# Performance work log

Measured on AMD Instinct MI355X. Metric: run time of the kernel, lower is better.

Reference implementation:

```python
import jax, jax.numpy as jnp
import numpy as np

N_NODES = 100000
N_EDGES = 1600000
C_IN, C_HID, C_OUT = 32, 32, 8
N_AGENTS = 1000


def _glorot(key, shape):
    fan_in, fan_out = shape[0], shape[1]
    lim = float(np.sqrt(6.0 / (fan_in + fan_out)))
    return jax.random.uniform(key, shape, jnp.float32, -lim, lim)


def setup_inputs() -> dict:
    key = jax.random.key(0)
    ks = jax.random.split(key, 16)
    x = jax.random.normal(ks[0], (N_NODES, C_IN), jnp.float32)
    edge_index = jax.random.randint(ks[1], (2, N_EDGES), 0, N_NODES, jnp.int64)
    d = {"x": x, "edge_index": edge_index}
    dims = [(C_IN, C_HID), (C_HID, C_HID), (C_HID, C_HID)]
    for i, (di, do) in enumerate(dims, start=1):
        d[f"W_l{i}"] = _glorot(ks[2 * i], (di, do))        # neighbor (aggregated) weight
        d[f"b_l{i}"] = jnp.zeros((do,), jnp.float32)
        d[f"W_r{i}"] = _glorot(ks[2 * i + 1], (di, do))    # root/self weight (no bias)
    d["W_out"] = _glorot(ks[10], (C_HID, C_OUT))
    d["b_out"] = jnp.zeros((C_OUT,), jnp.float32)
    return d


def _sage_conv(x, src, dst, W_l, b_l, W_r):
    # mean-aggregate neighbor features at destination nodes
    msg = x[src]                                               # [E, d] gather
    summed = jax.ops.segment_sum(msg, dst, num_segments=N_NODES)
    cnt = jax.ops.segment_sum(jnp.ones((src.shape[0],), x.dtype), dst,
                              num_segments=N_NODES)
    agg = summed / jnp.maximum(cnt, 1.0)[:, None]              # deg==0 -> 0
    return agg @ W_l + b_l + x @ W_r


def reference(x, edge_index, W_l1, b_l1, W_r1, W_l2, b_l2, W_r2,
              W_l3, b_l3, W_r3, W_out, b_out):
    src, dst = edge_index[0], edge_index[1]
    h = jax.nn.relu(_sage_conv(x, src, dst, W_l1, b_l1, W_r1))
    h = jax.nn.relu(_sage_conv(h, src, dst, W_l2, b_l2, W_r2))
    h = jax.nn.relu(_sage_conv(h, src, dst, W_l3, b_l3, W_r3))
    out = h @ W_out + b_out
    return out[:N_AGENTS]
```

## Files before the change

kernel.cpp:

```cpp
#include <hip/hip_runtime.h>
#include <hip/hip_bf16.h>

#define N_NODES 100000
#define N_EDGES 1600000
#define N_AGENTS 1000

#define NB 782
#define ABLK 512
#define CHUNK (N_EDGES / ABLK)
#define CONV_BLOCKS 3125

typedef short s16x8 __attribute__((ext_vector_type(8)));
typedef float f32x4 __attribute__((ext_vector_type(4)));

__device__ __forceinline__ unsigned short f2bf(float f) {
    unsigned u = __float_as_uint(f);
    u += 0x7fffu + ((u >> 16) & 1u);
    return (unsigned short)(u >> 16);
}
__device__ __forceinline__ float bflo(unsigned u) { return __uint_as_float(u << 16); }
__device__ __forceinline__ float bfhi(unsigned u) { return __uint_as_float(u & 0xffff0000u); }

__global__ __launch_bounds__(256) void hist_prep_kernel(
    const int* __restrict__ dst, int* __restrict__ partialT,
    const float* __restrict__ x, unsigned short* __restrict__ xb,
    const float* __restrict__ Wl1, const float* __restrict__ Wr1,
    const float* __restrict__ Wl2, const float* __restrict__ Wr2,
    const float* __restrict__ Wl3, const float* __restrict__ Wr3,
    unsigned short* __restrict__ Wcat)
{
    int b = blockIdx.x;
    if (b < ABLK) {
        __shared__ int hist[NB];
        for (int i = threadIdx.x; i < NB; i += 256) hist[i] = 0;
        __syncthreads();
        int beg = b * CHUNK;
        for (int e = beg + threadIdx.x; e < beg + CHUNK; e += 256)
            atomicAdd(&hist[dst[e] >> 7], 1);
        __syncthreads();
        for (int i = threadIdx.x; i < NB; i += 256) partialT[i * ABLK + b] = hist[i];
    } else if (b < ABLK + CONV_BLOCKS) {
        int i = (b - ABLK) * 256 + threadIdx.x;
        float4 v = ((const float4*)x)[i];
        ((ushort4*)xb)[i] = make_ushort4(f2bf(v.x), f2bf(v.y), f2bf(v.z), f2bf(v.w));
    } else {
        int gid = (b - ABLK - CONV_BLOCKS) * 256 + threadIdx.x;
        if (gid >= 3 * 2048) return;
        int L = gid >> 11, idx = gid & 2047;
        int k = idx >> 5, n = idx & 31;
        const float* Wl = (L == 0) ? Wl1 : (L == 1) ? Wl2 : Wl3;
        const float* Wr = (L == 0) ? Wr1 : (L == 1) ? Wr2 : Wr3;
        float v = (k < 32) ? Wl[k * 32 + n] : Wr[(k - 32) * 32 + n];
        Wcat[gid] = f2bf(v);
    }
}

__global__ __launch_bounds__(256) void bucket_prefix_kernel(
    const int* __restrict__ partialT, int* __restrict__ baseT, int* __restrict__ tot)
{
    int wave = threadIdx.x >> 6, lane = threadIdx.x & 63;
    int t = blockIdx.x * 4 + wave;
    if (t >= NB) return;
    const int4* p = (const int4*)(partialT + (size_t)t * ABLK);
    int4 u0 = p[lane * 2], u1 = p[lane * 2 + 1];
    int v0 = u0.x, v1 = u0.y, v2 = u0.z, v3 = u0.w;
    int v4 = u1.x, v5 = u1.y, v6 = u1.z, v7 = u1.w;
    int p0 = 0, p1 = v0, p2 = p1 + v1, p3 = p2 + v2;
    int p4 = p3 + v3, p5 = p4 + v4, p6 = p5 + v5, p7 = p6 + v6;
    int s = p7 + v7;
    int x = s;
    #pragma unroll
    for (int off = 1; off < 64; off <<= 1) {
        int y = __shfl_up(x, off);
        if (lane >= off) x += y;
    }
    int excl = x - s;
    int4* q = (int4*)(baseT + (size_t)t * ABLK);
    q[lane * 2]     = make_int4(excl + p0, excl + p1, excl + p2, excl + p3);
    q[lane * 2 + 1] = make_int4(excl + p4, excl + p5, excl + p6, excl + p7);
    if (lane == 63) tot[t] = x;
}

__global__ __launch_bounds__(1024) void total_scan_kernel(
    const int* __restrict__ tot, int* __restrict__ bstart)
{
    __shared__ int tmp[1024];
    int t = threadIdx.x;
    int v = (t < NB) ? tot[t] : 0;
    tmp[t] = v;
    __syncthreads();
    for (int off = 1; off < 1024; off <<= 1) {
        int u = (t >= off) ? tmp[t - off] : 0;
        __syncthreads();
        tmp[t] += u;
        __syncthreads();
    }
    if (t < NB) {
        bstart[t] = tmp[t] - v;
        if (t == NB - 1) bstart[NB] = tmp[t];
    }
}

__global__ __launch_bounds__(256) void bucket_scatter_kernel(
    const int* __restrict__ src, const int* __restrict__ dst,
    const int* __restrict__ baseT, const int* __restrict__ bstart,
    int* __restrict__ ebuf)
{
    __shared__ int cur[NB];
    int b = blockIdx.x;
    for (int i = threadIdx.x; i < NB; i += 256)
        cur[i] = bstart[i] + baseT[(size_t)i * ABLK + b];
    __syncthreads();
    int beg = b * CHUNK;
    for (int e = beg + threadIdx.x; e < beg + CHUNK; e += 256) {
        int d = dst[e];
        int slot = atomicAdd(&cur[d >> 7], 1);
        ebuf[slot] = src[e] | ((d & 127) << 17);
    }
}

__global__ __launch_bounds__(256) void bucket_csr_kernel(
    const int* __restrict__ bstart, const int* __restrict__ ebuf,
    int* __restrict__ rowptr, float* __restrict__ inv, int* __restrict__ esrc)
{
    __shared__ int hist[128], cur[128], tmp[256];
    int b = blockIdx.x;
    int t = threadIdx.x;
    int beg = bstart[b], end = bstart[b + 1];
    if (t < 128) hist[t] = 0;
    __syncthreads();
    for (int i = beg + t; i < end; i += 256)
        atomicAdd(&hist[(ebuf[i] >> 17) & 127], 1);
    __syncthreads();
    int v = (t < 128) ? hist[t] : 0;
    tmp[t] = v;
    __syncthreads();
    for (int off = 1; off < 256; off <<= 1) {
        int u = (t >= off) ? tmp[t - off] : 0;
        __syncthreads();
        tmp[t] += u;
        __syncthreads();
    }
    int excl = tmp[t] - v;
    int node = b * 128 + t;
    if (t < 128 && node < N_NODES) {
        rowptr[node] = beg + excl;
        inv[node] = 1.0f / fmaxf((float)v, 1.0f);
        cur[t] = beg + excl;
    }
    if (b == NB - 1 && t == 0) rowptr[N_NODES] = N_EDGES;
    __syncthreads();
    for (int i = beg + t; i < end; i += 256) {
        int p = ebuf[i];
        int slot = atomicAdd(&cur[(p >> 17) & 127], 1);
        esrc[slot] = p & 0x1FFFF;
    }
}

__global__ __launch_bounds__(256) void sage_fused_kernel(
    const int* __restrict__ rowptr, const int* __restrict__ esrc,
    const float* __restrict__ inv, const unsigned short* __restrict__ hb,
    const unsigned short* __restrict__ Wcat, const float* __restrict__ bl,
    const float* __restrict__ Wout, const float* __restrict__ bout,
    void* __restrict__ outp, int n_nodes, int final)
{
    __shared__ unsigned short sW[2048];
    __shared__ float sb[32];
    __shared__ unsigned short smean[64 * 40];
    __shared__ float sh3[64 * 33];
    __shared__ float sWo[256];
    __shared__ float sbo[8];

    int tid = threadIdx.x;
    ((uint4*)sW)[tid] = ((const uint4*)Wcat)[tid];
    if (tid < 32) sb[tid] = bl[tid];
    if (final) {
        sWo[tid] = Wout[tid];
        if (tid < 8) sbo[tid] = bout[tid];
    }

    int lane = tid & 63, wave = tid >> 6;

    int g = lane >> 2, q = lane & 3;
    int nodeA = blockIdx.x * 64 + wave * 16 + g;
    int beg = 0, end = 0;
    if (nodeA < n_nodes) { beg = rowptr[nodeA]; end = rowptr[nodeA + 1]; }
    float a0 = 0.f, a1 = 0.f, a2 = 0.f, a3 = 0.f;
    float a4 = 0.f, a5 = 0.f, a6 = 0.f, a7 = 0.f;
    int j = beg;
    for (; j + 1 < end; j += 2) {
        int s0 = esrc[j];
        int s1 = esrc[j + 1];
        uint4 u0 = *(const uint4*)(hb + s0 * 32 + q * 8);
        uint4 u1 = *(const uint4*)(hb + s1 * 32 + q * 8);
        a0 += bflo(u0.x); a1 += bfhi(u0.x);
        a2 += bflo(u0.y); a3 += bfhi(u0.y);
        a4 += bflo(u0.z); a5 += bfhi(u0.z);
        a6 += bflo(u0.w); a7 += bfhi(u0.w);
        a0 += bflo(u1.x); a1 += bfhi(u1.x);
        a2 += bflo(u1.y); a3 += bfhi(u1.y);
        a4 += bflo(u1.z); a5 += bfhi(u1.z);
        a6 += bflo(u1.w); a7 += bfhi(u1.w);
    }
    if (j < end) {
        int s = esrc[j];
        uint4 u = *(const uint4*)(hb + s * 32 + q * 8);
        a0 += bflo(u.x); a1 += bfhi(u.x);
        a2 += bflo(u.y); a3 += bfhi(u.y);
        a4 += bflo(u.z); a5 += bfhi(u.z);
        a6 += bflo(u.w); a7 += bfhi(u.w);
    }
    float iv = (nodeA < n_nodes) ? inv[nodeA] : 0.f;
    uint4 o;
    o.x = (unsigned)f2bf(a0 * iv) | ((unsigned)f2bf(a1 * iv) << 16);
    o.y = (unsigned)f2bf(a2 * iv) | ((unsigned)f2bf(a3 * iv) << 16);
    o.z = (unsigned)f2bf(a4 * iv) | ((unsigned)f2bf(a5 * iv) << 16);
    o.w = (unsigned)f2bf(a6 * iv) | ((unsigned)f2bf(a7 * iv) << 16);
    int mrow = wave * 16 + g;
    *(uint4*)&smean[mrow * 40 + q * 8] = o;
    __syncthreads();

    int l15 = lane & 15, quad = lane >> 4;
    s16x8 bf_[2][2];
    #pragma unroll
    for (int kt = 0; kt < 2; kt++)
        #pragma unroll
        for (int nt = 0; nt < 2; nt++)
            #pragma unroll
            for (int jj = 0; jj < 8; jj++) {
                int k = kt * 32 + quad * 8 + jj;
                bf_[kt][nt][jj] = (short)sW[k * 32 + l15 + nt * 16];
            }
    float bias0 = sb[l15], bias1 = sb[l15 + 16];

    int tilebase = blockIdx.x * 64 + wave * 16;
    int nodeD = tilebase + l15;
    int na = min(nodeD, n_nodes - 1);
    s16x8 am = *(const s16x8*)&smean[(wave * 16 + l15) * 40 + quad * 8];
    s16x8 as = *(const s16x8*)(hb + (size_t)na * 32 + quad * 8);
    f32x4 acc0 = {0.f, 0.f, 0.f, 0.f};
    f32x4 acc1 = {0.f, 0.f, 0.f, 0.f};
    acc0 = __builtin_amdgcn_mfma_f32_16x16x32_bf16(am, bf_[0][0], acc0, 0, 0, 0);
    acc0 = __builtin_amdgcn_mfma_f32_16x16x32_bf16(as, bf_[1][0], acc0, 0, 0, 0);
    acc1 = __builtin_amdgcn_mfma_f32_16x16x32_bf16(am, bf_[0][1], acc1, 0, 0, 0);
    acc1 = __builtin_amdgcn_mfma_f32_16x16x32_bf16(as, bf_[1][1], acc1, 0, 0, 0);

    if (!final) {
        #pragma unroll
        for (int r = 0; r < 4; r++) {
            int onode = tilebase + quad * 4 + r;
            if (onode < n_nodes) {
                ((unsigned short*)outp)[onode * 32 + l15]      = f2bf(fmaxf(acc0[r] + bias0, 0.f));
                ((unsigned short*)outp)[onode * 32 + l15 + 16] = f2bf(fmaxf(acc1[r] + bias1, 0.f));
            }
        }
    } else {
        #pragma unroll
        for (int r = 0; r < 4; r++) {
            int row = wave * 16 + quad * 4 + r;
            sh3[row * 33 + l15]      = fmaxf(acc0[r] + bias0, 0.f);
            sh3[row * 33 + l15 + 16] = fmaxf(acc1[r] + bias1, 0.f);
        }
        __syncthreads();
        #pragma unroll
        for (int i = tid; i < 512; i += 256) {
            int ln = i >> 3, c = i & 7;
            int gn = blockIdx.x * 64 + ln;
            if (gn < N_AGENTS) {
                float ov = sbo[c];
                #pragma unroll
                for (int k = 0; k < 32; k++) ov += sh3[ln * 33 + k] * sWo[k * 8 + c];
                ((float*)outp)[gn * 8 + c] = ov;
            }
        }
    }
}

extern "C" void kernel_launch(void* const* d_in, const int* in_sizes, int n_in,
                              void* d_out, int out_size, void* d_ws, size_t ws_size,
                              hipStream_t stream) {
    const float* x   = (const float*)d_in[0];
    const int* ei    = (const int*)d_in[1];
    const float* Wl1 = (const float*)d_in[2];
    const float* bl1 = (const float*)d_in[3];
    const float* Wr1 = (const float*)d_in[4];
    const float* Wl2 = (const float*)d_in[5];
    const float* bl2 = (const float*)d_in[6];
    const float* Wr2 = (const float*)d_in[7];
    const float* Wl3 = (const float*)d_in[8];
    const float* bl3 = (const float*)d_in[9];
    const float* Wr3 = (const float*)d_in[10];
    const float* Wout = (const float*)d_in[11];
    const float* bout = (const float*)d_in[12];
    float* out = (float*)d_out;

    const int* src = ei;
    const int* dst = ei + N_EDGES;

    char* ws = (char*)d_ws;
    int*   rowptr   = (int*)ws;                                ws += (size_t)(N_NODES + 8) * 4;
    float* inv      = (float*)ws;                              ws += (size_t)N_NODES * 4;
    int*   partialT = (int*)ws;                                ws += (size_t)NB * ABLK * 4;
    int*   baseT    = (int*)ws;                                ws += (size_t)NB * ABLK * 4;
    int*   tot      = (int*)ws;                                ws += 784 * 4;
    int*   bstart   = (int*)ws;                                ws += 784 * 4;
    int*   esrc     = (int*)ws;                                ws += (size_t)N_EDGES * 4;
    unsigned short* hXb   = (unsigned short*)ws;               ws += (size_t)N_NODES * 32 * 2;
    unsigned short* hAb   = (unsigned short*)ws;               ws += (size_t)N_NODES * 32 * 2;
    unsigned short* hBb   = (unsigned short*)ws;               ws += (size_t)N_NODES * 32 * 2;
    unsigned short* Wcat  = (unsigned short*)ws;               ws += 3 * 2048 * 2;
    int*   ebuf     = (int*)hAb;

    hist_prep_kernel<<<ABLK + CONV_BLOCKS + 24, 256, 0, stream>>>(
        dst, partialT, x, hXb, Wl1, Wr1, Wl2, Wr2, Wl3, Wr3, Wcat);
    bucket_prefix_kernel<<<(NB + 3) / 4, 256, 0, stream>>>(partialT, baseT, tot);
    total_scan_kernel<<<1, 1024, 0, stream>>>(tot, bstart);
    bucket_scatter_kernel<<<ABLK, 256, 0, stream>>>(src, dst, baseT, bstart, ebuf);
    bucket_csr_kernel<<<NB, 256, 0, stream>>>(bstart, ebuf, rowptr, inv, esrc);

    sage_fused_kernel<<<(N_NODES + 63) / 64, 256, 0, stream>>>(
        rowptr, esrc, inv, hXb, Wcat, bl1, Wout, bout, hAb, N_NODES, 0);
    sage_fused_kernel<<<(N_NODES + 63) / 64, 256, 0, stream>>>(
        rowptr, esrc, inv, hAb, Wcat + 2048, bl2, Wout, bout, hBb, N_NODES, 0);
    sage_fused_kernel<<<(N_AGENTS + 63) / 64, 256, 0, stream>>>(
        rowptr, esrc, inv, hBb, Wcat + 4096, bl3, Wout, bout, out, N_AGENTS, 1);
}
```

Baseline: 213.1 us.

## Sort nodes by in-degree to balance per-wave edge loops in SAGE layers

Builds a per-bucket degree histogram in the CSR kernel, scans it, and computes a permutation of nodes ordered by descending degree (capped at 63). The first two SAGE layers process nodes in this permuted order, so the 16 nodes in a wave have similar edge counts, reducing divergence and idle lanes in the gather loop. In exchange it adds two extra kernel launches and an indirection load, scatters output writes to non-contiguous rows, and lowers locality of the self-feature loads.

```diff
diff --git a/kernel.cpp b/kernel.cpp
--- a/kernel.cpp
+++ b/kernel.cpp
@@ -121,13 +121,15 @@
 
 __global__ __launch_bounds__(256) void bucket_csr_kernel(
     const int* __restrict__ bstart, const int* __restrict__ ebuf,
-    int* __restrict__ rowptr, float* __restrict__ inv, int* __restrict__ esrc)
-{
-    __shared__ int hist[128], cur[128], tmp[256];
+    int* __restrict__ rowptr, float* __restrict__ inv, int* __restrict__ esrc,
+    int* __restrict__ dbinP)
+{
+    __shared__ int hist[128], cur[128], tmp[256], dhist[64];
     int b = blockIdx.x;
     int t = threadIdx.x;
     int beg = bstart[b], end = bstart[b + 1];
     if (t < 128) hist[t] = 0;
+    if (t < 64) dhist[t] = 0;
     __syncthreads();
     for (int i = beg + t; i < end; i += 256)
         atomicAdd(&hist[(ebuf[i] >> 17) & 127], 1);
@@ -147,14 +149,71 @@
         rowptr[node] = beg + excl;
         inv[node] = 1.0f / fmaxf((float)v, 1.0f);
         cur[t] = beg + excl;
+        atomicAdd(&dhist[min(v, 63)], 1);
     }
     if (b == NB - 1 && t == 0) rowptr[N_NODES] = N_EDGES;
     __syncthreads();
+    if (t < 64) dbinP[b * 64 + t] = dhist[t];
     for (int i = beg + t; i < end; i += 256) {
         int p = ebuf[i];
         int slot = atomicAdd(&cur[(p >> 17) & 127], 1);
         esrc[slot] = p & 0x1FFFF;
     }
+}
+
+__global__ __launch_bounds__(256) void deg_scan_kernel(
+    const int* __restrict__ dbinP, int* __restrict__ dbaseP, int* __restrict__ dtot)
+{
+    int wave = threadIdx.x >> 6, lane = threadIdx.x & 63;
+    int bin = blockIdx.x * 4 + wave;
+    int vals[13];
+    int s = 0;
+    #pragma unroll
+    for (int it = 0; it < 13; it++) {
+        int b = lane * 13 + it;
+        int v = (b < NB) ? dbinP[b * 64 + bin] : 0;
+        vals[it] = v; s += v;
+    }
+    int x = s;
+    #pragma unroll
+    for (int off = 1; off < 64; off <<= 1) {
+        int y = __shfl_up(x, off);
+        if (lane >= off) x += y;
+    }
+    int run = x - s;
+    #pragma unroll
+    for (int it = 0; it < 13; it++) {
+        int b = lane * 13 + it;
+        if (b < NB) dbaseP[b * 64 + bin] = run;
+        run += vals[it];
+    }
+    if (lane == 63) dtot[bin] = x;
+}
+
+__global__ __launch_bounds__(256) void perm_place_kernel(
+    const int* __restrict__ rowptr, const int* __restrict__ dbinP,
+    const int* __restrict__ dbaseP, const int* __restrict__ dtot,
+    int* __restrict__ perm)
+{
+    __shared__ int lhist[2][64];
+    __shared__ int sstart[64];
+    int t = threadIdx.x;
+    if (t < 64) { lhist[0][t] = 0; lhist[1][t] = 0; }
+    if (t < 64) {
+        int s = 0;
+        for (int j = t + 1; j < 64; j++) s += dtot[j];
+        sstart[t] = s;
+    }
+    __syncthreads();
+    int i = blockIdx.x * 256 + t;
+    if (i >= N_NODES) return;
+    int deg = rowptr[i + 1] - rowptr[i];
+    int bin = min(deg, 63);
+    int half = t >> 7;
+    int rank = atomicAdd(&lhist[half][bin], 1);
+    int csrb = i >> 7;
+    int pos = sstart[bin] + dbaseP[csrb * 64 + bin] + rank;
+    perm[pos] = i;
 }
 
 __global__ __launch_bounds__(256) void sage_fused_kernel(
@@ -162,6 +221,7 @@
     const float* __restrict__ inv, const unsigned short* __restrict__ hb,
     const unsigned short* __restrict__ Wcat, const float* __restrict__ bl,
     const float* __restrict__ Wout, const float* __restrict__ bout,
+    const int* __restrict__ perm, int use_perm,
     void* __restrict__ outp, int n_nodes, int final)
 {
     __shared__ unsigned short sW[2048];
@@ -182,9 +242,11 @@
     int lane = tid & 63, wave = tid >> 6;
 
     int g = lane >> 2, q = lane & 3;
-    int nodeA = blockIdx.x * 64 + wave * 16 + g;
+    int idxA = blockIdx.x * 64 + wave * 16 + g;
+    int nodeA = -1;
+    if (idxA < n_nodes) nodeA = use_perm ? perm[idxA] : idxA;
     int beg = 0, end = 0;
-    if (nodeA < n_nodes) { beg = rowptr[nodeA]; end = rowptr[nodeA + 1]; }
+    if (nodeA >= 0) { beg = rowptr[nodeA]; end = rowptr[nodeA + 1]; }
     float a0 = 0.f, a1 = 0.f, a2 = 0.f, a3 = 0.f;
     float a4 = 0.f, a5 = 0.f, a6 = 0.f, a7 = 0.f;
     int j = beg;
@@ -210,7 +272,7 @@
         a4 += bflo(u.z); a5 += bfhi(u.z);
         a6 += bflo(u.w); a7 += bfhi(u.w);
     }
-    float iv = (nodeA < n_nodes) ? inv[nodeA] : 0.f;
+    float iv = (nodeA >= 0) ? inv[nodeA] : 0.f;
     uint4 o;
     o.x = (unsigned)f2bf(a0 * iv) | ((unsigned)f2bf(a1 * iv) << 16);
     o.y = (unsigned)f2bf(a2 * iv) | ((unsigned)f2bf(a3 * iv) << 16);
@@ -234,10 +296,11 @@
     float bias0 = sb[l15], bias1 = sb[l15 + 16];
 
     int tilebase = blockIdx.x * 64 + wave * 16;
-    int nodeD = tilebase + l15;
-    int na = min(nodeD, n_nodes - 1);
+    int idxD = tilebase + l15;
+    int pnode = 0;
+    if (idxD < n_nodes) pnode = use_perm ? perm[idxD] : idxD;
     s16x8 am = *(const s16x8*)&smean[(wave * 16 + l15) * 40 + quad * 8];
-    s16x8 as = *(const s16x8*)(hb + (size_t)na * 32 + quad * 8);
+    s16x8 as = *(const s16x8*)(hb + (size_t)pnode * 32 + quad * 8);
     f32x4 acc0 = {0.f, 0.f, 0.f, 0.f};
     f32x4 acc1 = {0.f, 0.f, 0.f, 0.f};
     acc0 = __builtin_amdgcn_mfma_f32_16x16x32_bf16(am, bf_[0][0], acc0, 0, 0, 0);
@@ -248,8 +311,9 @@
     if (!final) {
         #pragma unroll
         for (int r = 0; r < 4; r++) {
-            int onode = tilebase + quad * 4 + r;
-            if (onode < n_nodes) {
+            int oidx = tilebase + quad * 4 + r;
+            if (oidx < n_nodes) {
+                int onode = __shfl(pnode, quad * 4 + r);
                 ((unsigned short*)outp)[onode * 32 + l15]      = f2bf(fmaxf(acc0[r] + bias0, 0.f));
                 ((unsigned short*)outp)[onode * 32 + l15 + 16] = f2bf(fmaxf(acc1[r] + bias1, 0.f));
             }
@@ -309,6 +373,10 @@
     unsigned short* hAb   = (unsigned short*)ws;               ws += (size_t)N_NODES * 32 * 2;
     unsigned short* hBb   = (unsigned short*)ws;               ws += (size_t)N_NODES * 32 * 2;
     unsigned short* Wcat  = (unsigned short*)ws;               ws += 3 * 2048 * 2;
+    int*   dbinP    = (int*)ws;                                ws += (size_t)NB * 64 * 4;
+    int*   dbaseP   = (int*)ws;                                ws += (size_t)NB * 64 * 4;
+    int*   dtot     = (int*)ws;                                ws += 64 * 4;
+    int*   perm     = (int*)ws;                                ws += (size_t)N_NODES * 4;
     int*   ebuf     = (int*)hAb;
 
     hist_prep_kernel<<<ABLK + CONV_BLOCKS + 24, 256, 0, stream>>>(
@@ -316,12 +384,15 @@
     bucket_prefix_kernel<<<(NB + 3) / 4, 256, 0, stream>>>(partialT, baseT, tot);
     total_scan_kernel<<<1, 1024, 0, stream>>>(tot, bstart);
     bucket_scatter_kernel<<<ABLK, 256, 0, stream>>>(src, dst, baseT, bstart, ebuf);
-    bucket_csr_kernel<<<NB, 256, 0, stream>>>(bstart, ebuf, rowptr, inv, esrc);
+    bucket_csr_kernel<<<NB, 256, 0, stream>>>(bstart, ebuf, rowptr, inv, esrc, dbinP);
+
+    deg_scan_kernel<<<16, 256, 0, stream>>>(dbinP, dbaseP, dtot);
+    perm_place_kernel<<<(N_NODES + 255) / 256, 256, 0, stream>>>(rowptr, dbinP, dbaseP, dtot, perm);
 
     sage_fused_kernel<<<(N_NODES + 63) / 64, 256, 0, stream>>>(
-        rowptr, esrc, inv, hXb, Wcat, bl1, Wout, bout, hAb, N_NODES, 0);
+        rowptr, esrc, inv, hXb, Wcat, bl1, Wout, bout, perm, 1, hAb, N_NODES, 0);
     sage_fused_kernel<<<(N_NODES + 63) / 64, 256, 0, stream>>>(
-        rowptr, esrc, inv, hAb, Wcat + 2048, bl2, Wout, bout, hBb, N_NODES, 0);
+        rowptr, esrc, inv, hAb, Wcat + 2048, bl2, Wout, bout, perm, 1, hBb, N_NODES, 0);
     sage_fused_kernel<<<(N_AGENTS + 63) / 64, 256, 0, stream>>>(
-        rowptr, esrc, inv, hBb, Wcat + 4096, bl3, Wout, bout, out, N_AGENTS, 1);
-}
+        rowptr, esrc, inv, hBb, Wcat + 4096, bl3, Wout, bout, perm, 0, out, N_AGENTS, 1);
+}
```

Result: slower. 250.9 us (+17.7%).
